# Optimization experiments

Hardware: AMD Instinct MI355X
Metric: run time of the kernel (lower is better)

Reference implementation:

```python
import jax, jax.numpy as jnp
import numpy as np

RATIO = 4            # compress_ratio (overlap variant)
H, DH, ROPE = 16, 256, 64
NOPE = DH - ROPE
HI, DI = 32, 128     # indexer heads / head_dim
INOPE = DI - ROPE
TOPK = 256           # index_topk over compressed blocks
G, OLORA = 4, 512
THETA = 160000.0     # rope_theta when compress_ratio > 1
EPS = 1e-6
SCALE = DH ** -0.5
ISCALE = DI ** -0.5
NEG = -1e30


def rms(x, w):
    return (x * jax.lax.rsqrt(jnp.mean(x * x, -1, keepdims=True) + EPS)) * w


def rope_interleave(x, pos):
    # interleaved (GPT-NeoX-style pairs at even/odd lanes), matches rotary_mode='interleave'
    D = x.shape[-1]
    half = D // 2
    freq = THETA ** (-(jnp.arange(half, dtype=jnp.float32) * 2.0 / D))
    ang = pos.astype(jnp.float32)[:, None] * freq      # [T, half]
    cos, sin = jnp.cos(ang), jnp.sin(ang)
    if x.ndim == 3:
        cos, sin = cos[:, None, :], sin[:, None, :]
    x0, x1 = x[..., 0::2], x[..., 1::2]
    return jnp.stack([x0 * cos - x1 * sin, x0 * sin + x1 * cos], -1).reshape(x.shape)


def compress(x, wkv, wgate, ape, norm_w, d):
    # overlapping window compression: blocks of RATIO tokens, window = 2*RATIO (prev block's
    # first-half projections + own second-half), mean-pool + RMSNorm  -> [T/RATIO, d]
    T, dim = x.shape
    nb = T // RATIO
    xb = x.reshape(nb, RATIO, dim)
    kv = jnp.einsum('brd,de->bre', xb, wkv)            # [nb, RATIO, 2d]
    g = jax.nn.sigmoid(jnp.einsum('brd,de->bre', xb, wgate))
    kv = kv * g + ape                                   # ape: [RATIO, 2d] absolute-in-block pos emb
    win = jnp.zeros((nb, 2 * RATIO, d), kv.dtype)
    win = win.at[:, RATIO:].set(kv[:, :, d:])
    win = win.at[1:, :RATIO].set(kv[:-1, :, :d])        # overlap with previous block
    return rms(win.mean(1), norm_w)


def setup_inputs() -> dict:
    key = jax.random.key(0)
    T, DIM, QL, I = 2048, 2048, 1536, 8192
    ks = iter(jax.random.split(key, 32))
    def w(shape, s=0.02):
        return jax.random.normal(next(ks), shape, jnp.float32) * s
    return dict(
        hidden_states=jax.random.normal(next(ks), (T, DIM), jnp.float32),
        positions=jnp.arange(T, dtype=jnp.int32),
        ln1_w=jnp.ones((DIM,), jnp.float32), ln2_w=jnp.ones((DIM,), jnp.float32),
        wq_a=w((DIM, QL)), q_norm_w=jnp.ones((QL,), jnp.float32), wq_b=w((QL, H * DH)),
        comp_wkv=w((DIM, 2 * DH)), comp_wgate=w((DIM, 2 * DH)),
        comp_ape=w((RATIO, 2 * DH)), comp_norm_w=jnp.ones((DH,), jnp.float32),
        idx_wq_b=w((QL, HI * DI)), idx_weights_proj=w((DIM, HI)),
        icomp_wkv=w((DIM, 2 * DI)), icomp_wgate=w((DIM, 2 * DI)),
        icomp_ape=w((RATIO, 2 * DI)), icomp_norm_w=jnp.ones((DI,), jnp.float32),
        attn_sink=jnp.zeros((H,), jnp.float32),
        wo_a=w((G, OLORA, (H // G) * DH)), wo_b=w((G * OLORA, DIM)),
        gate_up_w=w((DIM, 2 * I)), down_w=w((I, DIM)),
    )


def reference(hidden_states, positions, ln1_w, ln2_w, wq_a, q_norm_w, wq_b,
              comp_wkv, comp_wgate, comp_ape, comp_norm_w,
              idx_wq_b, idx_weights_proj, icomp_wkv, icomp_wgate, icomp_ape, icomp_norm_w,
              attn_sink, wo_a, wo_b, gate_up_w, down_w):
    T, DIM = hidden_states.shape
    res = hidden_states
    x = rms(hidden_states, ln1_w)

    # ---- query path (low-rank) ----
    qr = rms(x @ wq_a, q_norm_w)                        # [T, QL]
    q = (qr @ wq_b).reshape(T, H, DH)
    q = jnp.concatenate([q[..., :NOPE], rope_interleave(q[..., NOPE:], positions)], -1)

    # ---- compressed shared KV (MLA-style single latent head) ----
    Sc = T // RATIO
    pos_c = (jnp.arange(Sc, dtype=jnp.int32) + 1) * RATIO - 1   # last position in each block
    kvc = compress(x, comp_wkv, comp_wgate, comp_ape, comp_norm_w, DH)   # [Sc, DH]
    kvc = jnp.concatenate([kvc[:, :NOPE], rope_interleave(kvc[:, NOPE:], pos_c)], -1)

    # ---- lightning indexer: topk compressed-token selection ----
    qi = (qr @ idx_wq_b).reshape(T, HI, DI)
    qi = jnp.concatenate([qi[..., :INOPE], rope_interleave(qi[..., INOPE:], positions)], -1)
    ki = compress(x, icomp_wkv, icomp_wgate, icomp_ape, icomp_norm_w, DI)  # [Sc, DI]
    ki = jnp.concatenate([ki[:, :INOPE], rope_interleave(ki[:, INOPE:], pos_c)], -1)
    iw = x @ idx_weights_proj                           # [T, HI] per-head index weights
    iscore = jnp.einsum('th,ths->ts', iw,
                        jax.nn.relu(jnp.einsum('thd,sd->ths', qi, ki)) * ISCALE)
    vis = pos_c[None, :] <= positions[:, None]          # block-causal visibility [T, Sc]
    idx = jax.lax.top_k(jnp.where(vis, iscore, NEG), TOPK)[1]
    sel = jnp.zeros((T, Sc), bool).at[jnp.arange(T)[:, None], idx].set(True)
    mask = vis & sel

    # ---- sparse attention over compressed KV with attention sink ----
    logits = jnp.einsum('thd,sd->ths', q, kvc) * SCALE  # [T, H, Sc]
    logits = jnp.where(mask[:, None, :], logits, NEG)
    logits = jnp.concatenate(
        [logits, jnp.broadcast_to(attn_sink[None, :, None], (T, H, 1))], -1)
    p = jax.nn.softmax(logits, axis=-1)[..., :Sc]       # drop sink column
    o = jnp.einsum('ths,sd->thd', p, kvc)               # [T, H, DH]

    # ---- grouped low-rank output projection ----
    og = o.reshape(T, G, (H // G) * DH)
    oa = jnp.einsum('tgf,gof->tgo', og, wo_a).reshape(T, G * OLORA)
    h = res + oa @ wo_b

    # ---- silu-gated MLP ----
    x2 = rms(h, ln2_w)
    gu = x2 @ gate_up_w
    I = gu.shape[-1] // 2
    return h + (jax.nn.silu(gu[:, :I]) * gu[:, I:]) @ down_w
```

## Files before the change

kernel.cpp:

```cpp
#include <hip/hip_runtime.h>
#include <hip/hip_bf16.h>
#include <cmath>

#define T 2048
#define DIM 2048
#define QL 1536
#define NH 16
#define DH 256
#define HI 32
#define DI 128
#define SC 512
#define II 8192
#define NCOMB 1664

typedef __hip_bfloat16 bf16;
typedef __attribute__((ext_vector_type(8))) short bf16x8;
typedef __attribute__((ext_vector_type(4))) float f32x4;

#define DEVI static __device__ __forceinline__

DEVI float b2f(short u){ union{unsigned x; float f;} v; v.x = ((unsigned)(unsigned short)u)<<16u; return v.f; }
DEVI short f2b(float x){ union{ __hip_bfloat16 b; short s;} v; v.b = __float2bfloat16(x); return v.s; }
DEVI bf16 f2bf(float x){ return __float2bfloat16(x); }
DEVI float sigm(float x){ return 1.f / (1.f + __expf(-x)); }

DEVI void gload16(const void* g, void* l) {
  __builtin_amdgcn_global_load_lds((const __attribute__((address_space(1))) void*)g,
                                   (__attribute__((address_space(3))) void*)l, 16, 0, 0);
}

DEVI float blockReduceSum(float v) {
  __shared__ float red[4];
  int lane = threadIdx.x & 63, w = threadIdx.x >> 6;
  #pragma unroll
  for (int m = 32; m >= 1; m >>= 1) v += __shfl_xor(v, m, 64);
  if (lane == 0) red[w] = v;
  __syncthreads();
  int nw = blockDim.x >> 6;
  float s = 0.f;
  for (int i = 0; i < nw; i++) s += red[i];
  return s;
}

__global__ void k_transpose(const float* __restrict__ in, bf16* __restrict__ out, int R, int C) {
  __shared__ float tile[32][33];
  int c0 = blockIdx.x * 32, r0 = blockIdx.y * 32;
  int tx = threadIdx.x, ty = threadIdx.y;
  #pragma unroll
  for (int i = 0; i < 4; i++)
    tile[ty + i*8][tx] = in[(size_t)(r0 + ty + i*8) * C + c0 + tx];
  __syncthreads();
  #pragma unroll
  for (int i = 0; i < 4; i++)
    out[(size_t)(c0 + ty + i*8) * R + r0 + tx] = f2bf(tile[tx][ty + i*8]);
}

__global__ void k_convert(const float* __restrict__ in, bf16* __restrict__ out, int n) {
  for (int i = blockIdx.x*256 + threadIdx.x; i < n; i += gridDim.x*256) out[i] = f2bf(in[i]);
}

__global__ __launch_bounds__(256) void k_rms(const float* __restrict__ in, const float* __restrict__ w,
                                             bf16* __restrict__ out, int D) {
  int t = blockIdx.x;
  const float* row = in + (size_t)t * D;
  float ss = 0.f;
  for (int j = threadIdx.x; j < D/4; j += 256) {
    float4 v = ((const float4*)row)[j];
    ss += v.x*v.x + v.y*v.y + v.z*v.z + v.w*v.w;
  }
  ss = blockReduceSum(ss);
  float rs = rsqrtf(ss / (float)D + 1e-6f);
  for (int j = threadIdx.x; j < D/4; j += 256) {
    float4 v = ((const float4*)row)[j];
    float4 ww = ((const float4*)w)[j];
    union { short s[4]; uint2 u; } pk;
    pk.s[0] = f2b(v.x*rs*ww.x); pk.s[1] = f2b(v.y*rs*ww.y);
    pk.s[2] = f2b(v.z*rs*ww.z); pk.s[3] = f2b(v.w*rs*ww.w);
    ((uint2*)(out + (size_t)t*D))[j] = pk.u;
  }
}

__global__ void k_rope_table(const int* __restrict__ positions, float* __restrict__ tabc, float* __restrict__ tabs) {
  int row = blockIdx.x * 8 + threadIdx.y;
  int i = threadIdx.x;
  if (row >= T + SC) return;
  float pos = (row < T) ? (float)positions[row] : (float)(4*(row - T) + 3);
  float freq = powf(160000.0f, -(float)i / 32.0f);
  float ang = pos * freq;
  tabc[(size_t)row*32 + i] = cosf(ang);
  tabs[(size_t)row*32 + i] = sinf(ang);
}

__global__ __launch_bounds__(256) void k_rope_apply(const float* __restrict__ in, bf16* __restrict__ out,
                                                    const float* __restrict__ tabc, const float* __restrict__ tabs,
                                                    int Hn, int Dn, int nope) {
  int t = blockIdx.x;
  int hd = blockIdx.y * 256 + threadIdx.x;
  int h = hd / Dn, d = hd - h*Dn;
  const float* row = in + (size_t)t * Hn * Dn;
  float val;
  if (d < nope) val = row[hd];
  else {
    int k = d - nope, i = k >> 1;
    float x0 = row[h*Dn + nope + 2*i], x1 = row[h*Dn + nope + 2*i + 1];
    float c = tabc[(size_t)t*32 + i], s = tabs[(size_t)t*32 + i];
    val = (k & 1) ? (x0*s + x1*c) : (x0*c - x1*s);
  }
  out[(size_t)t*Hn*Dn + hd] = f2bf(val);
}

template<int BF16_OUT, int RES>
__global__ __launch_bounds__(256) void k_gemm(
    const bf16* __restrict__ A, int lda, long long aZ,
    const bf16* __restrict__ BT, long long bZ,
    void* __restrict__ Cout, int ldc, int cZ,
    const float* __restrict__ resid, int K)
{
  __shared__ bf16 sA[128*32];
  __shared__ bf16 sB[128*32];
  const int tid = threadIdx.x;
  const int w = tid >> 6, lane = tid & 63;
  const int wr = w >> 1, wc = w & 1;
  const int kid = lane >> 4, lr = lane & 15;
  const int bm = blockIdx.y, bn = blockIdx.x, bz = blockIdx.z;
  const bf16* Ab = A + aZ*bz + (size_t)bm*128*lda;
  const bf16* Bb = BT + bZ*bz + (size_t)bn*128*K;
  f32x4 acc[4][4] = {};
  const int chb = w*128 + lane;
  for (int k0 = 0; k0 < K; k0 += 32) {
    #pragma unroll
    for (int i = 0; i < 2; i++) {
      int c = chb + i*64;
      gload16(Ab + (size_t)(c>>2)*lda + k0 + (c&3)*8, sA + (size_t)(w*128 + i*64)*8);
      gload16(Bb + (size_t)(c>>2)*K   + k0 + (c&3)*8, sB + (size_t)(w*128 + i*64)*8);
    }
    __syncthreads();
    bf16x8 a[4], b[4];
    #pragma unroll
    for (int m = 0; m < 4; m++) a[m] = *(const bf16x8*)(sA + (wr*64 + m*16 + lr)*32 + kid*8);
    #pragma unroll
    for (int n = 0; n < 4; n++) b[n] = *(const bf16x8*)(sB + (wc*64 + n*16 + lr)*32 + kid*8);
    #pragma unroll
    for (int m = 0; m < 4; m++)
      #pragma unroll
      for (int n = 0; n < 4; n++)
        acc[m][n] = __builtin_amdgcn_mfma_f32_16x16x32_bf16(a[m], b[n], acc[m][n], 0, 0, 0);
    __syncthreads();
  }
  const int rb = bm*128 + wr*64 + kid*4;
  const int cb = cZ*bz + bn*128 + wc*64 + lr;
  #pragma unroll
  for (int m = 0; m < 4; m++)
    #pragma unroll
    for (int n = 0; n < 4; n++)
      #pragma unroll
      for (int r = 0; r < 4; r++) {
        int row = rb + m*16 + r;
        int col = cb + n*16;
        float v = acc[m][n][r];
        if (RES) v += resid[(size_t)row*ldc + col];
        if (BF16_OUT) ((bf16*)Cout)[(size_t)row*ldc + col] = f2bf(v);
        else          ((float*)Cout)[(size_t)row*ldc + col] = v;
      }
}

__global__ __launch_bounds__(256) void k_iscore(
    const bf16* __restrict__ QI,
    const bf16* __restrict__ KI,
    const float* __restrict__ comb,
    float* __restrict__ iscore)
{
  __shared__ bf16 sA[128*32];
  __shared__ bf16 sB[128*32];
  __shared__ float sc[512];
  const int tid = threadIdx.x;
  const int w = tid >> 6, lane = tid & 63;
  const int wr = w >> 1, wc = w & 1;
  const int kid = lane >> 4, lr = lane & 15;
  const int bm = blockIdx.y, bn = blockIdx.x;
  for (int i = tid; i < 512; i += 256) sc[i] = 0.f;
  const bf16* Ab = QI + (size_t)bm*128*DI;
  const bf16* Bb = KI + (size_t)bn*128*DI;
  f32x4 acc[4][4] = {};
  const int chb = w*128 + lane;
  for (int k0 = 0; k0 < DI; k0 += 32) {
    #pragma unroll
    for (int i = 0; i < 2; i++) {
      int c = chb + i*64;
      gload16(Ab + (size_t)(c>>2)*DI + k0 + (c&3)*8, sA + (size_t)(w*128 + i*64)*8);
      gload16(Bb + (size_t)(c>>2)*DI + k0 + (c&3)*8, sB + (size_t)(w*128 + i*64)*8);
    }
    __syncthreads();
    bf16x8 a[4], b[4];
    #pragma unroll
    for (int m = 0; m < 4; m++) a[m] = *(const bf16x8*)(sA + (wr*64 + m*16 + lr)*32 + kid*8);
    #pragma unroll
    for (int n = 0; n < 4; n++) b[n] = *(const bf16x8*)(sB + (wc*64 + n*16 + lr)*32 + kid*8);
    #pragma unroll
    for (int m = 0; m < 4; m++)
      #pragma unroll
      for (int n = 0; n < 4; n++)
        acc[m][n] = __builtin_amdgcn_mfma_f32_16x16x32_bf16(a[m], b[n], acc[m][n], 0, 0, 0);
    __syncthreads();
  }
  #pragma unroll
  for (int m = 0; m < 4; m++) {
    int rowl = wr*64 + m*16 + kid*4;
    #pragma unroll
    for (int r = 0; r < 4; r++) {
      int grow = bm*128 + rowl + r;
      int tt = grow >> 5, h = grow & 31;
      float wgt = comb[(size_t)tt*NCOMB + 1536 + h] * 0.08838834764831845f;
      #pragma unroll
      for (int n = 0; n < 4; n++) {
        float v = fmaxf(acc[m][n][r], 0.f) * wgt;
        atomicAdd(&sc[((rowl + r) >> 5)*128 + wc*64 + n*16 + lr], v);
      }
    }
  }
  __syncthreads();
  for (int i = tid; i < 512; i += 256)
    iscore[(size_t)(bm*4 + (i >> 7))*SC + bn*128 + (i & 127)] = sc[i];
}

__global__ __launch_bounds__(256) void k_combine_c(
    const float* __restrict__ comb, const float* __restrict__ ape, const float* __restrict__ normw,
    const float* __restrict__ tabc, const float* __restrict__ tabs,
    bf16* __restrict__ kvc, bf16* __restrict__ kvcT)
{
  const int b = blockIdx.x, j = threadIdx.x;
  float acc = 0.f;
  #pragma unroll
  for (int r = 0; r < 4; r++) {
    if (b > 0) {
      size_t tt = (size_t)(4*(b-1)+r) * NCOMB;
      acc += comb[tt + j] * sigm(comb[tt + 512 + j]) + ape[r*512 + j];
    }
    size_t t2 = (size_t)(4*b+r) * NCOMB;
    acc += comb[t2 + 256 + j] * sigm(comb[t2 + 512 + 256 + j]) + ape[r*512 + 256 + j];
  }
  acc *= 0.125f;
  float ss = blockReduceSum(acc*acc);
  float rs = rsqrtf(ss * (1.f/256.f) + 1e-6f);
  float nv = acc * rs * normw[j];
  __shared__ float sh[256];
  sh[j] = nv;
  __syncthreads();
  float outv;
  if (j < 192) outv = nv;
  else {
    int k = j - 192, i = k >> 1;
    float x0 = sh[192 + 2*i], x1 = sh[193 + 2*i];
    float c = tabc[(size_t)(T + b)*32 + i], sn = tabs[(size_t)(T + b)*32 + i];
    outv = (k & 1) ? (x0*sn + x1*c) : (x0*c - x1*sn);
  }
  kvc[(size_t)b*DH + j] = f2bf(outv);
  kvcT[(size_t)j*SC + b] = f2bf(outv);
}

__global__ __launch_bounds__(128) void k_combine_i(
    const float* __restrict__ comb, const float* __restrict__ ape, const float* __restrict__ normw,
    const float* __restrict__ tabc, const float* __restrict__ tabs,
    bf16* __restrict__ ki)
{
  const int b = blockIdx.x, j = threadIdx.x;
  float acc = 0.f;
  #pragma unroll
  for (int r = 0; r < 4; r++) {
    if (b > 0) {
      size_t tt = (size_t)(4*(b-1)+r) * NCOMB;
      acc += comb[tt + 1024 + j] * sigm(comb[tt + 1280 + j]) + ape[r*256 + j];
    }
    size_t t2 = (size_t)(4*b+r) * NCOMB;
    acc += comb[t2 + 1024 + 128 + j] * sigm(comb[t2 + 1280 + 128 + j]) + ape[r*256 + 128 + j];
  }
  acc *= 0.125f;
  float ss = blockReduceSum(acc*acc);
  float rs = rsqrtf(ss * (1.f/128.f) + 1e-6f);
  float nv = acc * rs * normw[j];
  __shared__ float sh[128];
  sh[j] = nv;
  __syncthreads();
  float outv;
  if (j < 64) outv = nv;
  else {
    int k = j - 64, i = k >> 1;
    float x0 = sh[64 + 2*i], x1 = sh[64 + 2*i + 1];
    float c = tabc[(size_t)(T + b)*32 + i], sn = tabs[(size_t)(T + b)*32 + i];
    outv = (k & 1) ? (x0*sn + x1*c) : (x0*c - x1*sn);
  }
  ki[(size_t)b*DI + j] = f2bf(outv);
}

__global__ __launch_bounds__(256) void k_topk(const float* __restrict__ iscore,
                                              const int* __restrict__ positions,
                                              float* __restrict__ thresh) {
  const int t = blockIdx.x;
  int pos = positions[t];
  int nv = (pos + 1) >> 2; if (nv > SC) nv = SC;
  if (nv <= 256) { if (threadIdx.x == 0) thresh[t] = -3e38f; return; }
  __shared__ float arr[512];
  for (int i = threadIdx.x; i < 512; i += 256)
    arr[i] = (i < nv) ? iscore[(size_t)t*SC + i] : -1e30f;
  __syncthreads();
  for (int k = 2; k <= 512; k <<= 1)
    for (int j = k >> 1; j > 0; j >>= 1) {
      for (int idx = threadIdx.x; idx < 512; idx += 256) {
        int ixj = idx ^ j;
        if (ixj > idx) {
          bool up = ((idx & k) == 0);
          float a = arr[idx], b = arr[ixj];
          if (up ? (a < b) : (a > b)) { arr[idx] = b; arr[ixj] = a; }
        }
      }
      __syncthreads();
    }
  if (threadIdx.x == 0) thresh[t] = arr[255];
}

__global__ __launch_bounds__(256) void k_attn(
    const bf16* __restrict__ q, const bf16* __restrict__ kvc, const bf16* __restrict__ kvcT,
    const float* __restrict__ iscore, const float* __restrict__ thresh,
    const int* __restrict__ positions, const float* __restrict__ sink,
    bf16* __restrict__ o)
{
  const int t = blockIdx.x;
  const int tid = threadIdx.x, w = tid >> 6, lane = tid & 63;
  const int kid = lane >> 4, lr = lane & 15;
  __shared__ bf16 pl[16*528];
  __shared__ float redm[4][16], reds[4][16];
  int pos = positions[t];
  int nv = (pos + 1) >> 2; if (nv > SC) nv = SC;
  float th = thresh[t];
  bf16x8 aq[8];
  const bf16* qrow = q + (size_t)t*(NH*DH) + lr*DH + kid*8;
  #pragma unroll
  for (int ks = 0; ks < 8; ks++) aq[ks] = *(const bf16x8*)(qrow + ks*32);
  f32x4 acc[8] = {};
  const int s0 = w*128;
  if (s0 < nv) {
    #pragma unroll
    for (int ks = 0; ks < 8; ks++) {
      bf16x8 bq[8];
      #pragma unroll
      for (int n = 0; n < 8; n++)
        bq[n] = *(const bf16x8*)(kvc + (size_t)(s0 + n*16 + lr)*DH + ks*32 + kid*8);
      #pragma unroll
      for (int n = 0; n < 8; n++)
        acc[n] = __builtin_amdgcn_mfma_f32_16x16x32_bf16(aq[ks], bq[n], acc[n], 0, 0, 0);
    }
  }
  float p[8][4];
  float mx[4] = {-3e38f, -3e38f, -3e38f, -3e38f};
  #pragma unroll
  for (int n = 0; n < 8; n++) {
    int s = s0 + n*16 + lr;
    bool keep = (s < nv) && (iscore[(size_t)t*SC + s] >= th);
    #pragma unroll
    for (int r = 0; r < 4; r++) {
      float v = keep ? acc[n][r] * 0.0625f : -1e30f;
      p[n][r] = v;
      mx[r] = fmaxf(mx[r], v);
    }
  }
  #pragma unroll
  for (int m2 = 1; m2 <= 8; m2 <<= 1)
    #pragma unroll
    for (int r = 0; r < 4; r++) mx[r] = fmaxf(mx[r], __shfl_xor(mx[r], m2, 64));
  if (lr == 0) {
    #pragma unroll
    for (int r = 0; r < 4; r++) redm[w][kid*4 + r] = mx[r];
  }
  __syncthreads();
  float M[4], sm[4];
  #pragma unroll
  for (int r = 0; r < 4; r++) {
    int h = kid*4 + r;
    float m = fmaxf(fmaxf(redm[0][h], redm[1][h]), fmaxf(redm[2][h], redm[3][h]));
    M[r] = fmaxf(m, sink[h]);
    sm[r] = 0.f;
  }
  #pragma unroll
  for (int n = 0; n < 8; n++)
    #pragma unroll
    for (int r = 0; r < 4; r++) {
      float e = __expf(p[n][r] - M[r]);
      p[n][r] = e;
      sm[r] += e;
    }
  #pragma unroll
  for (int m2 = 1; m2 <= 8; m2 <<= 1)
    #pragma unroll
    for (int r = 0; r < 4; r++) sm[r] += __shfl_xor(sm[r], m2, 64);
  if (lr == 0) {
    #pragma unroll
    for (int r = 0; r < 4; r++) reds[w][kid*4 + r] = sm[r];
  }
  __syncthreads();
  float inv[4];
  #pragma unroll
  for (int r = 0; r < 4; r++) {
    int h = kid*4 + r;
    float den = reds[0][h] + reds[1][h] + reds[2][h] + reds[3][h] + __expf(sink[h] - M[r]);
    inv[r] = 1.f / den;
  }
  #pragma unroll
  for (int n = 0; n < 8; n++)
    #pragma unroll
    for (int r = 0; r < 4; r++)
      pl[(kid*4 + r)*528 + s0 + n*16 + lr] = f2bf(p[n][r] * inv[r]);
  __syncthreads();
  int nch = (nv + 31) >> 5; if (nch > 16) nch = 16;
  f32x4 oacc[4] = {};
  for (int ks = 0; ks < nch; ks++) {
    bf16x8 ap = *(const bf16x8*)(pl + lr*528 + ks*32 + kid*8);
    #pragma unroll
    for (int n = 0; n < 4; n++) {
      bf16x8 bv = *(const bf16x8*)(kvcT + (size_t)(w*64 + n*16 + lr)*SC + ks*32 + kid*8);
      oacc[n] = __builtin_amdgcn_mfma_f32_16x16x32_bf16(ap, bv, oacc[n], 0, 0, 0);
    }
  }
  #pragma unroll
  for (int n = 0; n < 4; n++)
    #pragma unroll
    for (int r = 0; r < 4; r++)
      o[(size_t)t*(NH*DH) + (kid*4 + r)*DH + w*64 + n*16 + lr] = f2bf(oacc[n][r]);
}

__global__ __launch_bounds__(256) void k_act(const bf16* __restrict__ gu, bf16* __restrict__ a) {
  size_t i = (size_t)blockIdx.x*256 + threadIdx.x;
  size_t t = i >> 10;
  size_t c = (i & 1023) * 8;
  bf16x8 g8 = *(const bf16x8*)(gu + t*16384 + c);
  bf16x8 u8 = *(const bf16x8*)(gu + t*16384 + 8192 + c);
  union { short s[8]; bf16x8 v; } outp;
  #pragma unroll
  for (int j = 0; j < 8; j++) {
    float g = b2f(g8[j]), u = b2f(u8[j]);
    outp.s[j] = f2b((g / (1.f + __expf(-g))) * u);
  }
  *(bf16x8*)(a + t*8192 + c) = outp.v;
}

extern "C" void kernel_launch(void* const* d_in, const int* in_sizes, int n_in,
                              void* d_out, int out_size, void* d_ws, size_t ws_size,
                              hipStream_t stream) {
  const float* hidden        = (const float*)d_in[0];
  const int*   positions     = (const int*)  d_in[1];
  const float* ln1_w         = (const float*)d_in[2];
  const float* ln2_w         = (const float*)d_in[3];
  const float* wq_a          = (const float*)d_in[4];
  const float* q_norm_w      = (const float*)d_in[5];
  const float* wq_b          = (const float*)d_in[6];
  const float* comp_wkv      = (const float*)d_in[7];
  const float* comp_wgate    = (const float*)d_in[8];
  const float* comp_ape      = (const float*)d_in[9];
  const float* comp_norm_w   = (const float*)d_in[10];
  const float* idx_wq_b      = (const float*)d_in[11];
  const float* idx_wproj     = (const float*)d_in[12];
  const float* icomp_wkv     = (const float*)d_in[13];
  const float* icomp_wgate   = (const float*)d_in[14];
  const float* icomp_ape     = (const float*)d_in[15];
  const float* icomp_norm_w  = (const float*)d_in[16];
  const float* attn_sink     = (const float*)d_in[17];
  const float* wo_a          = (const float*)d_in[18];
  const float* wo_b          = (const float*)d_in[19];
  const float* gate_up_w     = (const float*)d_in[20];
  const float* down_w        = (const float*)d_in[21];
  float* outp = (float*)d_out;

  char* p = (char*)d_ws;
  auto take = [&](size_t n) { char* r = p; p += (n + 255) & ~(size_t)255; return r; };
  bf16* wq_aT    = (bf16*)take((size_t)QL*DIM*2);
  bf16* wq_bT    = (bf16*)take((size_t)4096*QL*2);
  bf16* idx_wq_bT= (bf16*)take((size_t)4096*QL*2);
  bf16* WcombT   = (bf16*)take((size_t)NCOMB*DIM*2);
  bf16* wo_a_bf  = (bf16*)take((size_t)4*512*1024*2);
  bf16* wo_bT    = (bf16*)take((size_t)DIM*DIM*2);
  bf16* gate_upT = (bf16*)take((size_t)2*II*DIM*2);
  bf16* downT    = (bf16*)take((size_t)DIM*II*2);
  bf16* x_bf     = (bf16*)take((size_t)T*DIM*2);
  char* R1 = take((size_t)T*16384*2);
  float* qtmp  = (float*)R1;
  bf16*  q_bf  = (bf16*)(R1 + (size_t)33554432);
  bf16*  qi_bf = (bf16*)(R1 + (size_t)50331648);
  bf16*  o_bf  = (bf16*)R1;
  bf16*  oa_bf = (bf16*)(R1 + (size_t)16777216);
  bf16*  gu    = (bf16*)R1;
  char* R2 = take((size_t)36700160);
  float* qx     = (float*)R2;
  bf16*  qr     = (bf16*)(R2 + (size_t)12582912);
  float* comb   = (float*)(R2 + (size_t)18874368);
  float* iscore = (float*)(R2 + (size_t)32505856);
  bf16*  x2     = (bf16*)(R2 + (size_t)18874368);
  bf16*  a_bf   = (bf16*)R2;
  float* hbuf = (float*)take((size_t)T*DIM*4);
  bf16* kvc   = (bf16*)take((size_t)SC*DH*2);
  bf16* kvcT  = (bf16*)take((size_t)DH*SC*2);
  bf16* ki    = (bf16*)take((size_t)SC*DI*2);
  float* tabc = (float*)take((size_t)(T+SC)*32*4);
  float* tabs = (float*)take((size_t)(T+SC)*32*4);
  float* thr  = (float*)take((size_t)T*4);

  dim3 tb(32, 8);
  k_transpose<<<dim3(QL/32, DIM/32), tb, 0, stream>>>(wq_a, wq_aT, DIM, QL);
  k_transpose<<<dim3(4096/32, QL/32), tb, 0, stream>>>(wq_b, wq_bT, QL, 4096);
  k_transpose<<<dim3(4096/32, QL/32), tb, 0, stream>>>(idx_wq_b, idx_wq_bT, QL, 4096);
  k_transpose<<<dim3(512/32, DIM/32), tb, 0, stream>>>(comp_wkv,   WcombT + (size_t)0*DIM,    DIM, 512);
  k_transpose<<<dim3(512/32, DIM/32), tb, 0, stream>>>(comp_wgate, WcombT + (size_t)512*DIM,  DIM, 512);
  k_transpose<<<dim3(256/32, DIM/32), tb, 0, stream>>>(icomp_wkv,  WcombT + (size_t)1024*DIM, DIM, 256);
  k_transpose<<<dim3(256/32, DIM/32), tb, 0, stream>>>(icomp_wgate,WcombT + (size_t)1280*DIM, DIM, 256);
  k_transpose<<<dim3(32/32, DIM/32), tb, 0, stream>>>(idx_wproj,   WcombT + (size_t)1536*DIM, DIM, 32);
  k_transpose<<<dim3(DIM/32, DIM/32), tb, 0, stream>>>(wo_b, wo_bT, DIM, DIM);
  k_transpose<<<dim3(16384/32, DIM/32), tb, 0, stream>>>(gate_up_w, gate_upT, DIM, 16384);
  k_transpose<<<dim3(DIM/32, II/32), tb, 0, stream>>>(down_w, downT, II, DIM);
  k_convert<<<2048, 256, 0, stream>>>(wo_a, wo_a_bf, 4*512*1024);
  k_rope_table<<<(T + SC + 7)/8, tb, 0, stream>>>(positions, tabc, tabs);

  k_rms<<<T, 256, 0, stream>>>(hidden, ln1_w, x_bf, DIM);
  k_gemm<0,0><<<dim3(QL/128, T/128), 256, 0, stream>>>(x_bf, DIM, 0, wq_aT, 0, qx, QL, 0, nullptr, DIM);
  k_rms<<<T, 256, 0, stream>>>(qx, q_norm_w, qr, QL);
  k_gemm<0,0><<<dim3(4096/128, T/128), 256, 0, stream>>>(qr, QL, 0, wq_bT, 0, qtmp, 4096, 0, nullptr, QL);
  k_rope_apply<<<dim3(T, 16), 256, 0, stream>>>(qtmp, q_bf, tabc, tabs, NH, DH, 192);
  k_gemm<0,0><<<dim3(4096/128, T/128), 256, 0, stream>>>(qr, QL, 0, idx_wq_bT, 0, qtmp, 4096, 0, nullptr, QL);
  k_rope_apply<<<dim3(T, 16), 256, 0, stream>>>(qtmp, qi_bf, tabc, tabs, HI, DI, 64);
  k_gemm<0,0><<<dim3(NCOMB/128, T/128), 256, 0, stream>>>(x_bf, DIM, 0, WcombT, 0, comb, NCOMB, 0, nullptr, DIM);
  k_combine_c<<<SC, 256, 0, stream>>>(comb, comp_ape, comp_norm_w, tabc, tabs, kvc, kvcT);
  k_combine_i<<<SC, 128, 0, stream>>>(comb, icomp_ape, icomp_norm_w, tabc, tabs, ki);
  k_iscore<<<dim3(4, 512), 256, 0, stream>>>(qi_bf, ki, comb, iscore);
  k_topk<<<T, 256, 0, stream>>>(iscore, positions, thr);
  k_attn<<<T, 256, 0, stream>>>(q_bf, kvc, kvcT, iscore, thr, positions, attn_sink, o_bf);
  k_gemm<1,0><<<dim3(4, T/128, 4), 256, 0, stream>>>(o_bf, NH*DH, 1024, wo_a_bf, (long long)512*1024,
                                                     oa_bf, DIM, 512, nullptr, 1024);
  k_gemm<0,1><<<dim3(DIM/128, T/128), 256, 0, stream>>>(oa_bf, DIM, 0, wo_bT, 0, hbuf, DIM, 0, hidden, DIM);
  k_rms<<<T, 256, 0, stream>>>(hbuf, ln2_w, x2, DIM);
  k_gemm<1,0><<<dim3(16384/128, T/128), 256, 0, stream>>>(x2, DIM, 0, gate_upT, 0, gu, 16384, 0, nullptr, DIM);
  k_act<<<(int)((size_t)T*II/8/256), 256, 0, stream>>>(gu, a_bf);
  k_gemm<0,1><<<dim3(DIM/128, T/128), 256, 0, stream>>>(a_bf, II, 0, downT, 0, outp, DIM, 0, hbuf, II);
}
```

Before: 1.439 ms.

## Vectorize transposes, fuse bf16 q output with rope, split-K small GEMMs, add XCD swizzle

```diff
diff --git a/kernel.cpp b/kernel.cpp
--- a/kernel.cpp
+++ b/kernel.cpp
@@ -42,7 +42,32 @@
   return s;
 }
 
-__global__ void k_transpose(const float* __restrict__ in, bf16* __restrict__ out, int R, int C) {
+__global__ __launch_bounds__(256) void k_transpose64(const float* __restrict__ in, bf16* __restrict__ out,
+                                                     int R, int C) {
+  __shared__ float tile[64][65];
+  int c0 = blockIdx.x * 64, r0 = blockIdx.y * 64;
+  int tid = threadIdx.x;
+  int cg = tid & 15, rr = tid >> 4;
+  #pragma unroll
+  for (int rb = 0; rb < 4; rb++) {
+    int row = rb*16 + rr;
+    float4 v = *(const float4*)(in + (size_t)(r0+row)*C + c0 + cg*4);
+    tile[row][cg*4+0] = v.x; tile[row][cg*4+1] = v.y;
+    tile[row][cg*4+2] = v.z; tile[row][cg*4+3] = v.w;
+  }
+  __syncthreads();
+  int cc = tid >> 3, rblk = tid & 7;
+  #pragma unroll
+  for (int ci = 0; ci < 2; ci++) {
+    int c = ci*32 + cc;
+    union { short s[8]; bf16x8 v; } pk;
+    #pragma unroll
+    for (int i = 0; i < 8; i++) pk.s[i] = f2b(tile[rblk*8+i][c]);
+    *(bf16x8*)(out + (size_t)(c0+c)*R + r0 + rblk*8) = pk.v;
+  }
+}
+
+__global__ void k_transpose32(const float* __restrict__ in, bf16* __restrict__ out, int R, int C) {
   __shared__ float tile[32][33];
   int c0 = blockIdx.x * 32, r0 = blockIdx.y * 32;
   int tx = threadIdx.x, ty = threadIdx.y;
@@ -91,29 +116,37 @@
   tabs[(size_t)row*32 + i] = sinf(ang);
 }
 
-__global__ __launch_bounds__(256) void k_rope_apply(const float* __restrict__ in, bf16* __restrict__ out,
-                                                    const float* __restrict__ tabc, const float* __restrict__ tabs,
-                                                    int Hn, int Dn, int nope) {
+__global__ __launch_bounds__(256) void k_rope8(const bf16* __restrict__ in, bf16* __restrict__ out,
+                                               const float* __restrict__ tabc, const float* __restrict__ tabs,
+                                               int HD, int Dn, int nope) {
   int t = blockIdx.x;
-  int hd = blockIdx.y * 256 + threadIdx.x;
-  int h = hd / Dn, d = hd - h*Dn;
-  const float* row = in + (size_t)t * Hn * Dn;
-  float val;
-  if (d < nope) val = row[hd];
+  int v8 = blockIdx.y*256 + threadIdx.x;
+  int hd0 = v8*8;
+  if (hd0 >= HD) return;
+  int h = hd0 / Dn, d0 = hd0 - h*Dn;
+  bf16x8 x = *(const bf16x8*)(in + (size_t)t*HD + hd0);
+  union { short s[8]; bf16x8 v; } o;
+  if (d0 < nope) { o.v = x; }
   else {
-    int k = d - nope, i = k >> 1;
-    float x0 = row[h*Dn + nope + 2*i], x1 = row[h*Dn + nope + 2*i + 1];
-    float c = tabc[(size_t)t*32 + i], s = tabs[(size_t)t*32 + i];
-    val = (k & 1) ? (x0*s + x1*c) : (x0*c - x1*s);
-  }
-  out[(size_t)t*Hn*Dn + hd] = f2bf(val);
-}
-
-template<int BF16_OUT, int RES>
+    int i0 = (d0 - nope) >> 1;
+    float4 c4 = *(const float4*)(tabc + (size_t)t*32 + i0);
+    float4 s4 = *(const float4*)(tabs + (size_t)t*32 + i0);
+    float cA[4] = {c4.x,c4.y,c4.z,c4.w}, sA[4] = {s4.x,s4.y,s4.z,s4.w};
+    #pragma unroll
+    for (int pI = 0; pI < 4; pI++) {
+      float x0 = b2f(x[2*pI]), x1 = b2f(x[2*pI+1]);
+      o.s[2*pI]   = f2b(x0*cA[pI] - x1*sA[pI]);
+      o.s[2*pI+1] = f2b(x0*sA[pI] + x1*cA[pI]);
+    }
+  }
+  *(bf16x8*)(out + (size_t)t*HD + hd0) = o.v;
+}
+
+template<int BF16_OUT, int RES, int SWZ>
 __global__ __launch_bounds__(256) void k_gemm(
     const bf16* __restrict__ A, int lda, long long aZ,
-    const bf16* __restrict__ BT, long long bZ,
-    void* __restrict__ Cout, int ldc, int cZ,
+    const bf16* __restrict__ BT, int ldb, long long bZ,
+    void* __restrict__ Cout, int ldc, long long cOffZ,
     const float* __restrict__ resid, int K)
 {
   __shared__ bf16 sA[128*32];
@@ -122,9 +155,17 @@
   const int w = tid >> 6, lane = tid & 63;
   const int wr = w >> 1, wc = w & 1;
   const int kid = lane >> 4, lr = lane & 15;
-  const int bm = blockIdx.y, bn = blockIdx.x, bz = blockIdx.z;
+  int bn = blockIdx.x, bm = blockIdx.y, bz = blockIdx.z;
+  if (SWZ) {
+    int gx = gridDim.x, gy = gridDim.y;
+    int nwg = gx*gy*gridDim.z;
+    int lin = (bz*gy + bm)*gx + bn;
+    int q = nwg >> 3, r = nwg & 7, x = lin & 7, s = lin >> 3;
+    int m = (x < r) ? x*(q+1) + s : r*(q+1) + (x-r)*q + s;
+    bn = m % gx; int tmp = m / gx; bm = tmp % gy; bz = tmp / gy;
+  }
   const bf16* Ab = A + aZ*bz + (size_t)bm*128*lda;
-  const bf16* Bb = BT + bZ*bz + (size_t)bn*128*K;
+  const bf16* Bb = BT + bZ*bz + (size_t)bn*128*ldb;
   f32x4 acc[4][4] = {};
   const int chb = w*128 + lane;
   for (int k0 = 0; k0 < K; k0 += 32) {
@@ -132,7 +173,7 @@
     for (int i = 0; i < 2; i++) {
       int c = chb + i*64;
       gload16(Ab + (size_t)(c>>2)*lda + k0 + (c&3)*8, sA + (size_t)(w*128 + i*64)*8);
-      gload16(Bb + (size_t)(c>>2)*K   + k0 + (c&3)*8, sB + (size_t)(w*128 + i*64)*8);
+      gload16(Bb + (size_t)(c>>2)*ldb + k0 + (c&3)*8, sB + (size_t)(w*128 + i*64)*8);
     }
     __syncthreads();
     bf16x8 a[4], b[4];
@@ -148,20 +189,31 @@
     __syncthreads();
   }
   const int rb = bm*128 + wr*64 + kid*4;
-  const int cb = cZ*bz + bn*128 + wc*64 + lr;
+  const int cb = bn*128 + wc*64 + lr;
   #pragma unroll
   for (int m = 0; m < 4; m++)
     #pragma unroll
     for (int n = 0; n < 4; n++)
       #pragma unroll
       for (int r = 0; r < 4; r++) {
-        int row = rb + m*16 + r;
-        int col = cb + n*16;
+        long long idx = cOffZ*bz + (long long)(rb + m*16 + r)*ldc + cb + n*16;
         float v = acc[m][n][r];
-        if (RES) v += resid[(size_t)row*ldc + col];
-        if (BF16_OUT) ((bf16*)Cout)[(size_t)row*ldc + col] = f2bf(v);
-        else          ((float*)Cout)[(size_t)row*ldc + col] = v;
+        if (RES) v += resid[idx];
+        if (BF16_OUT) ((bf16*)Cout)[idx] = f2bf(v);
+        else          ((float*)Cout)[idx] = v;
       }
+}
+
+__global__ __launch_bounds__(256) void k_redN(const float* __restrict__ resid, const float* __restrict__ part,
+                                              int nparts, long long stride, float* __restrict__ out, int n4) {
+  int i = blockIdx.x*256 + threadIdx.x;
+  if (i >= n4) return;
+  float4 a = ((const float4*)resid)[i];
+  for (int z = 0; z < nparts; z++) {
+    float4 pv = ((const float4*)(part + stride*z))[i];
+    a.x += pv.x; a.y += pv.y; a.z += pv.z; a.w += pv.w;
+  }
+  ((float4*)out)[i] = a;
 }
 
 __global__ __launch_bounds__(256) void k_iscore(
@@ -481,12 +533,12 @@
   bf16* downT    = (bf16*)take((size_t)DIM*II*2);
   bf16* x_bf     = (bf16*)take((size_t)T*DIM*2);
   char* R1 = take((size_t)T*16384*2);
-  float* qtmp  = (float*)R1;
-  bf16*  q_bf  = (bf16*)(R1 + (size_t)33554432);
-  bf16*  qi_bf = (bf16*)(R1 + (size_t)50331648);
-  bf16*  o_bf  = (bf16*)R1;
-  bf16*  oa_bf = (bf16*)(R1 + (size_t)16777216);
-  bf16*  gu    = (bf16*)R1;
+  bf16*  qtmp_bf = (bf16*)R1;
+  bf16*  q_bf    = (bf16*)(R1 + (size_t)16777216);
+  bf16*  qi_bf   = (bf16*)(R1 + (size_t)33554432);
+  bf16*  o_bf    = (bf16*)R1;
+  bf16*  oa_bf   = (bf16*)(R1 + (size_t)33554432);
+  bf16*  gu      = (bf16*)R1;
   char* R2 = take((size_t)36700160);
   float* qx     = (float*)R2;
   bf16*  qr     = (bf16*)(R2 + (size_t)12582912);
@@ -501,40 +553,45 @@
   float* tabc = (float*)take((size_t)(T+SC)*32*4);
   float* tabs = (float*)take((size_t)(T+SC)*32*4);
   float* thr  = (float*)take((size_t)T*4);
-
-  dim3 tb(32, 8);
-  k_transpose<<<dim3(QL/32, DIM/32), tb, 0, stream>>>(wq_a, wq_aT, DIM, QL);
-  k_transpose<<<dim3(4096/32, QL/32), tb, 0, stream>>>(wq_b, wq_bT, QL, 4096);
-  k_transpose<<<dim3(4096/32, QL/32), tb, 0, stream>>>(idx_wq_b, idx_wq_bT, QL, 4096);
-  k_transpose<<<dim3(512/32, DIM/32), tb, 0, stream>>>(comp_wkv,   WcombT + (size_t)0*DIM,    DIM, 512);
-  k_transpose<<<dim3(512/32, DIM/32), tb, 0, stream>>>(comp_wgate, WcombT + (size_t)512*DIM,  DIM, 512);
-  k_transpose<<<dim3(256/32, DIM/32), tb, 0, stream>>>(icomp_wkv,  WcombT + (size_t)1024*DIM, DIM, 256);
-  k_transpose<<<dim3(256/32, DIM/32), tb, 0, stream>>>(icomp_wgate,WcombT + (size_t)1280*DIM, DIM, 256);
-  k_transpose<<<dim3(32/32, DIM/32), tb, 0, stream>>>(idx_wproj,   WcombT + (size_t)1536*DIM, DIM, 32);
-  k_transpose<<<dim3(DIM/32, DIM/32), tb, 0, stream>>>(wo_b, wo_bT, DIM, DIM);
-  k_transpose<<<dim3(16384/32, DIM/32), tb, 0, stream>>>(gate_up_w, gate_upT, DIM, 16384);
-  k_transpose<<<dim3(DIM/32, II/32), tb, 0, stream>>>(down_w, downT, II, DIM);
+  float* partial4 = (float*)gate_upT;
+  float* partial2 = (float*)wq_aT;
+
+  k_transpose64<<<dim3(QL/64, DIM/64), 256, 0, stream>>>(wq_a, wq_aT, DIM, QL);
+  k_transpose64<<<dim3(4096/64, QL/64), 256, 0, stream>>>(wq_b, wq_bT, QL, 4096);
+  k_transpose64<<<dim3(4096/64, QL/64), 256, 0, stream>>>(idx_wq_b, idx_wq_bT, QL, 4096);
+  k_transpose64<<<dim3(512/64, DIM/64), 256, 0, stream>>>(comp_wkv,   WcombT + (size_t)0*DIM,    DIM, 512);
+  k_transpose64<<<dim3(512/64, DIM/64), 256, 0, stream>>>(comp_wgate, WcombT + (size_t)512*DIM,  DIM, 512);
+  k_transpose64<<<dim3(256/64, DIM/64), 256, 0, stream>>>(icomp_wkv,  WcombT + (size_t)1024*DIM, DIM, 256);
+  k_transpose64<<<dim3(256/64, DIM/64), 256, 0, stream>>>(icomp_wgate,WcombT + (size_t)1280*DIM, DIM, 256);
+  k_transpose32<<<dim3(1, DIM/32), dim3(32,8), 0, stream>>>(idx_wproj, WcombT + (size_t)1536*DIM, DIM, 32);
+  k_transpose64<<<dim3(DIM/64, DIM/64), 256, 0, stream>>>(wo_b, wo_bT, DIM, DIM);
+  k_transpose64<<<dim3(16384/64, DIM/64), 256, 0, stream>>>(gate_up_w, gate_upT, DIM, 16384);
+  k_transpose64<<<dim3(DIM/64, II/64), 256, 0, stream>>>(down_w, downT, II, DIM);
   k_convert<<<2048, 256, 0, stream>>>(wo_a, wo_a_bf, 4*512*1024);
-  k_rope_table<<<(T + SC + 7)/8, tb, 0, stream>>>(positions, tabc, tabs);
+  k_rope_table<<<(T + SC + 7)/8, dim3(32,8), 0, stream>>>(positions, tabc, tabs);
 
   k_rms<<<T, 256, 0, stream>>>(hidden, ln1_w, x_bf, DIM);
-  k_gemm<0,0><<<dim3(QL/128, T/128), 256, 0, stream>>>(x_bf, DIM, 0, wq_aT, 0, qx, QL, 0, nullptr, DIM);
+  k_gemm<0,0,1><<<dim3(QL/128, T/128), 256, 0, stream>>>(x_bf, DIM, 0, wq_aT, DIM, 0, qx, QL, 0, nullptr, DIM);
   k_rms<<<T, 256, 0, stream>>>(qx, q_norm_w, qr, QL);
-  k_gemm<0,0><<<dim3(4096/128, T/128), 256, 0, stream>>>(qr, QL, 0, wq_bT, 0, qtmp, 4096, 0, nullptr, QL);
-  k_rope_apply<<<dim3(T, 16), 256, 0, stream>>>(qtmp, q_bf, tabc, tabs, NH, DH, 192);
-  k_gemm<0,0><<<dim3(4096/128, T/128), 256, 0, stream>>>(qr, QL, 0, idx_wq_bT, 0, qtmp, 4096, 0, nullptr, QL);
-  k_rope_apply<<<dim3(T, 16), 256, 0, stream>>>(qtmp, qi_bf, tabc, tabs, HI, DI, 64);
-  k_gemm<0,0><<<dim3(NCOMB/128, T/128), 256, 0, stream>>>(x_bf, DIM, 0, WcombT, 0, comb, NCOMB, 0, nullptr, DIM);
+  k_gemm<1,0,1><<<dim3(4096/128, T/128), 256, 0, stream>>>(qr, QL, 0, wq_bT, QL, 0, qtmp_bf, 4096, 0, nullptr, QL);
+  k_rope8<<<dim3(T, 2), 256, 0, stream>>>(qtmp_bf, q_bf, tabc, tabs, 4096, DH, 192);
+  k_gemm<1,0,1><<<dim3(4096/128, T/128), 256, 0, stream>>>(qr, QL, 0, idx_wq_bT, QL, 0, qtmp_bf, 4096, 0, nullptr, QL);
+  k_rope8<<<dim3(T, 2), 256, 0, stream>>>(qtmp_bf, qi_bf, tabc, tabs, 4096, DI, 64);
+  k_gemm<0,0,1><<<dim3(NCOMB/128, T/128), 256, 0, stream>>>(x_bf, DIM, 0, WcombT, DIM, 0, comb, NCOMB, 0, nullptr, DIM);
   k_combine_c<<<SC, 256, 0, stream>>>(comb, comp_ape, comp_norm_w, tabc, tabs, kvc, kvcT);
   k_combine_i<<<SC, 128, 0, stream>>>(comb, icomp_ape, icomp_norm_w, tabc, tabs, ki);
   k_iscore<<<dim3(4, 512), 256, 0, stream>>>(qi_bf, ki, comb, iscore);
   k_topk<<<T, 256, 0, stream>>>(iscore, positions, thr);
   k_attn<<<T, 256, 0, stream>>>(q_bf, kvc, kvcT, iscore, thr, positions, attn_sink, o_bf);
-  k_gemm<1,0><<<dim3(4, T/128, 4), 256, 0, stream>>>(o_bf, NH*DH, 1024, wo_a_bf, (long long)512*1024,
-                                                     oa_bf, DIM, 512, nullptr, 1024);
-  k_gemm<0,1><<<dim3(DIM/128, T/128), 256, 0, stream>>>(oa_bf, DIM, 0, wo_bT, 0, hbuf, DIM, 0, hidden, DIM);
+  k_gemm<1,0,1><<<dim3(4, T/128, 4), 256, 0, stream>>>(o_bf, NH*DH, 1024, wo_a_bf, 1024, (long long)512*1024,
+                                                       oa_bf, DIM, 512, nullptr, 1024);
+  k_gemm<0,0,1><<<dim3(DIM/128, T/128, 2), 256, 0, stream>>>(oa_bf, DIM, 1024, wo_bT, DIM, 1024,
+                                                             partial2, DIM, (long long)T*DIM, nullptr, 1024);
+  k_redN<<<(T*DIM/4 + 255)/256, 256, 0, stream>>>(hidden, partial2, 2, (long long)T*DIM, hbuf, T*DIM/4);
   k_rms<<<T, 256, 0, stream>>>(hbuf, ln2_w, x2, DIM);
-  k_gemm<1,0><<<dim3(16384/128, T/128), 256, 0, stream>>>(x2, DIM, 0, gate_upT, 0, gu, 16384, 0, nullptr, DIM);
+  k_gemm<1,0,1><<<dim3(16384/128, T/128), 256, 0, stream>>>(x2, DIM, 0, gate_upT, DIM, 0, gu, 16384, 0, nullptr, DIM);
   k_act<<<(int)((size_t)T*II/8/256), 256, 0, stream>>>(gu, a_bf);
-  k_gemm<0,1><<<dim3(DIM/128, T/128), 256, 0, stream>>>(a_bf, II, 0, downT, 0, outp, DIM, 0, hbuf, II);
-}
+  k_gemm<0,0,1><<<dim3(DIM/128, T/128, 4), 256, 0, stream>>>(a_bf, II, 2048, downT, II, 2048,
+                                                             partial4, DIM, (long long)T*DIM, nullptr, 2048);
+  k_redN<<<(T*DIM/4 + 255)/256, 256, 0, stream>>>(hbuf, partial4, 4, (long long)T*DIM, outp, T*DIM/4);
+}
```

Result: faster. 1.340 ms (-6.9%).
